# Kernel optimization log

Hardware: AMD Instinct MI355X
Metric: run time of the kernel (lower is better)

The kernel has to match this reference:

```python
import jax, jax.numpy as jnp
import numpy as np

V = 4096      # num codes (vocab)
D = 128       # embedding dim
K = 3         # diffusion scales
H = 4         # attn heads
FF = 128      # ff hidden
L = 2         # attn layers
NVIS = 8192   # visits
MAXC = 32     # max codes per visit
PAD = 0


def logmap0(x):
    # Poincare ball (c=1) log map at origin: artanh(||x||) * x / ||x||
    eps = 1e-7
    norm = jnp.linalg.norm(x, axis=-1, keepdims=True)
    norm_c = jnp.clip(norm, eps, 1.0 - 1e-5)
    return jnp.arctanh(norm_c) * x / jnp.maximum(norm, eps)


def layer_norm(x, g, b, eps=1e-5):
    m = jnp.mean(x, axis=-1, keepdims=True)
    v = jnp.mean((x - m) ** 2, axis=-1, keepdims=True)
    return (x - m) * jax.lax.rsqrt(v + eps) * g + b


def attn_block(x, Wqkv, bqkv, Wo, bo, W1, b1, W2, b2, g1, be1, g2, be2):
    # x: [V, D] (batch of 1, squeezed)
    hd = D // H
    qkv = x @ Wqkv.T + bqkv                      # [V, 3D]
    q, k, v = jnp.split(qkv, 3, axis=-1)
    q = q.reshape(V, H, hd)
    k = k.reshape(V, H, hd)
    v = v.reshape(V, H, hd)
    scores = jnp.einsum('shd,thd->hst', q, k) / np.sqrt(hd).astype(x.dtype)
    a = jax.nn.softmax(scores, axis=-1)          # [H, V, V]
    o = jnp.einsum('hst,thd->shd', a, v).reshape(V, D)
    attn_out = o @ Wo.T + bo
    x = layer_norm(x + attn_out, g1, be1)
    ff = jax.nn.gelu(x @ W1.T + b1) @ W2.T + b2
    return layer_norm(x + ff, g2, be2)


def setup_inputs() -> dict:
    key = jax.random.key(0)
    ks = jax.random.split(key, 20)
    inp = {}
    inp['visits'] = jax.random.randint(ks[0], (NVIS, MAXC), 0, V)
    # hyperbolic points inside unit ball
    inp['X_hyp'] = jax.random.normal(ks[1], (V, D), jnp.float32) * 0.01
    inp['kernels'] = jax.random.normal(ks[2], (K, V, V), jnp.float32) / V
    inp['proj_W'] = jax.random.normal(ks[3], (D, K * D), jnp.float32) * 0.05
    inp['proj_b'] = jnp.zeros((D,), jnp.float32)
    s = 0.05
    inp['Wqkv'] = jax.random.normal(ks[4], (L, 3 * D, D), jnp.float32) * s
    inp['bqkv'] = jnp.zeros((L, 3 * D), jnp.float32)
    inp['Wo'] = jax.random.normal(ks[5], (L, D, D), jnp.float32) * s
    inp['bo'] = jnp.zeros((L, D), jnp.float32)
    inp['W1'] = jax.random.normal(ks[6], (L, FF, D), jnp.float32) * s
    inp['b1'] = jnp.zeros((L, FF), jnp.float32)
    inp['W2'] = jax.random.normal(ks[7], (L, D, FF), jnp.float32) * s
    inp['b2'] = jnp.zeros((L, D), jnp.float32)
    inp['ln1_g'] = jnp.ones((L, D), jnp.float32)
    inp['ln1_b'] = jnp.zeros((L, D), jnp.float32)
    inp['ln2_g'] = jnp.ones((L, D), jnp.float32)
    inp['ln2_b'] = jnp.zeros((L, D), jnp.float32)
    return inp


def reference(visits, X_hyp, kernels, proj_W, proj_b, Wqkv, bqkv, Wo, bo,
              W1, b1, W2, b2, ln1_g, ln1_b, ln2_g, ln2_b):
    # ---- hyperbolic graph diffusion ----
    Z0 = logmap0(X_hyp)                              # [V, D]
    Z_scales = jnp.einsum('kuv,vd->ukd', kernels, Z0)  # [V, K, D]
    Z_cat = Z_scales.reshape(V, K * D)
    H_ = Z_cat @ proj_W.T + proj_b                   # [V, D]
    # ---- global self-attention stack ----
    for l in range(L):
        H_ = attn_block(H_, Wqkv[l], bqkv[l], Wo[l], bo[l],
                        W1[l], b1[l], W2[l], b2[l],
                        ln1_g[l], ln1_b[l], ln2_g[l], ln2_b[l])
    # ---- per-visit masked mean pooling (segment mean) ----
    mask = (visits != PAD)                           # [NVIS, MAXC]
    gathered = H_[visits] * mask[..., None]          # [NVIS, MAXC, D]
    cnt = jnp.sum(mask, axis=-1, keepdims=True).astype(H_.dtype)
    summed = jnp.sum(gathered, axis=1)               # [NVIS, D]
    return jnp.where(cnt > 0, summed / jnp.maximum(cnt, 1.0), 0.0)
```

## Files before the change

kernel.cpp:

```cpp
#include <hip/hip_runtime.h>
#include <hip/hip_bf16.h>
#include <math.h>

#define VN 4096
#define DIM 128
#define KS 3
#define NH 4
#define HD 32
#define NVIS 8192
#define MAXC 32
#define KTOT (KS*VN)

typedef unsigned short u16;
typedef __attribute__((ext_vector_type(8))) short short8;
typedef __attribute__((ext_vector_type(4))) float f32x4;
typedef __attribute__((ext_vector_type(4))) float f4v;

__device__ __forceinline__ u16 f2b(float f){
  union { float f; unsigned u; } c; c.f = f;
  unsigned u = c.u;
  return (u16)((u + 0x7fffu + ((u >> 16) & 1u)) >> 16);
}
__device__ __forceinline__ float b2f(u16 x){
  union { float f; unsigned u; } c; c.u = ((unsigned)x) << 16; return c.f;
}
__device__ __forceinline__ unsigned cvt2(float lo, float hi){
  unsigned r;
  asm("v_cvt_pk_bf16_f32 %0, %1, %2" : "=v"(r) : "v"(lo), "v"(hi));
  return r;
}
#define MFMA16(a,b,c) __builtin_amdgcn_mfma_f32_16x16x32_bf16((a),(b),(c),0,0,0)

__global__ __launch_bounds__(256) void k_logmap(const float* __restrict__ xh, u16* __restrict__ z0){
  __shared__ float xs[64][132];
  __shared__ float part[4][64];
  __shared__ float sscale[64];
  int t = threadIdx.x;
  int v0 = blockIdx.x * 64;
  #pragma unroll
  for(int i=0;i<8;i++){
    int id = t + 256*i; int e = id*4; int r = e>>7; int c = e&127;
    float4 u = *(const float4*)&xh[(size_t)(v0+r)*DIM + c];
    xs[r][c+0]=u.x; xs[r][c+1]=u.y; xs[r][c+2]=u.z; xs[r][c+3]=u.w;
  }
  __syncthreads();
  int r = t & 63, q = t >> 6;
  float p = 0.f;
  #pragma unroll
  for(int c=0;c<32;c++){ float x = xs[r][q*32+c]; p += x*x; }
  part[q][r] = p;
  __syncthreads();
  if(t < 64){
    float ss = part[0][t]+part[1][t]+part[2][t]+part[3][t];
    float n = sqrtf(ss);
    float nc = fminf(fmaxf(n, 1e-7f), 1.0f - 1e-5f);
    sscale[t] = atanhf(nc) / fmaxf(n, 1e-7f);
  }
  __syncthreads();
  #pragma unroll
  for(int i=0;i<8;i++){
    int id = t + 256*i; int e = id*4; int rr = e>>7; int cc = e&127;
    float s = sscale[rr];
    uint2 o = { cvt2(xs[rr][cc+0]*s, xs[rr][cc+1]*s),
                cvt2(xs[rr][cc+2]*s, xs[rr][cc+3]*s) };
    *(uint2*)&z0[(size_t)(v0+rr)*DIM + cc] = o;
  }
}

template<bool AF32, bool BF32>
__device__ __forceinline__ void gemm_k128_t(const void* __restrict__ Agv, int lda,
                                            const void* __restrict__ Bgv, int ldb,
                                            u16 (*As)[128*72], u16 (*Bs)[128*72], f32x4 (&acc)[2][8]){
  int t = threadIdx.x;
  int w=t>>6, lane=t&63, l15=lane&15, quad=lane>>4;
  #pragma unroll
  for(int s=0;s<2;s++)
    #pragma unroll
    for(int n=0;n<8;n++) acc[s][n] = (f32x4){0.f,0.f,0.f,0.f};

  float4 af[4][2]; uint4 ai[4];
  float4 bf[4][2]; uint4 bi[4];

  auto LOAD = [&](int kb){
    #pragma unroll
    for(int i=0;i<4;i++){
      int id = t + 256*i; int row = id>>3, c8 = id&7;
      if constexpr(AF32){
        const float* Ag = (const float*)Agv;
        af[i][0] = *(const float4*)&Ag[(size_t)row*lda + kb + c8*8];
        af[i][1] = *(const float4*)&Ag[(size_t)row*lda + kb + c8*8 + 4];
      } else {
        const u16* Ag = (const u16*)Agv;
        ai[i] = *(const uint4*)&Ag[(size_t)row*lda + kb + c8*8];
      }
      if constexpr(BF32){
        const float* Bg = (const float*)Bgv;
        bf[i][0] = *(const float4*)&Bg[(size_t)row*ldb + kb + c8*8];
        bf[i][1] = *(const float4*)&Bg[(size_t)row*ldb + kb + c8*8 + 4];
      } else {
        const u16* Bg = (const u16*)Bgv;
        bi[i] = *(const uint4*)&Bg[(size_t)row*ldb + kb + c8*8];
      }
    }
  };
  auto COMMIT = [&](u16* Ad, u16* Bd){
    #pragma unroll
    for(int i=0;i<4;i++){
      int id = t + 256*i; int row = id>>3, c8 = id&7;
      if constexpr(AF32){
        uint4 p = { cvt2(af[i][0].x, af[i][0].y), cvt2(af[i][0].z, af[i][0].w),
                    cvt2(af[i][1].x, af[i][1].y), cvt2(af[i][1].z, af[i][1].w) };
        *(uint4*)&Ad[row*72 + c8*8] = p;
      } else {
        *(uint4*)&Ad[row*72 + c8*8] = ai[i];
      }
      if constexpr(BF32){
        uint4 q = { cvt2(bf[i][0].x, bf[i][0].y), cvt2(bf[i][0].z, bf[i][0].w),
                    cvt2(bf[i][1].x, bf[i][1].y), cvt2(bf[i][1].z, bf[i][1].w) };
        *(uint4*)&Bd[row*72 + c8*8] = q;
      } else {
        *(uint4*)&Bd[row*72 + c8*8] = bi[i];
      }
    }
  };
  auto COMPUTE = [&](const u16* Asb, const u16* Bsb){
    #pragma unroll
    for(int ks=0; ks<2; ks++){
      short8 a[2], b[8];
      #pragma unroll
      for(int s=0;s<2;s++) a[s] = *(const short8*)&Asb[(w*32+s*16+l15)*72 + (ks*4+quad)*8];
      #pragma unroll
      for(int n=0;n<8;n++)  b[n] = *(const short8*)&Bsb[(n*16+l15)*72 + (ks*4+quad)*8];
      #pragma unroll
      for(int s=0;s<2;s++)
        #pragma unroll
        for(int n=0;n<8;n++) acc[s][n] = MFMA16(a[s], b[n], acc[s][n]);
    }
  };

  LOAD(0);  COMMIT(As[0], Bs[0]);  __syncthreads();
  LOAD(64); COMPUTE(As[0], Bs[0]); COMMIT(As[1], Bs[1]); __syncthreads();
  COMPUTE(As[1], Bs[1]);
}

__global__ __launch_bounds__(256) void k_gproj(const float* __restrict__ projW, const u16* __restrict__ z0,
                                               u16* __restrict__ gbuf){
  __shared__ u16 As[2][128*72], Bs[2][128*72];
  int kb = blockIdx.x >> 5, vt = blockIdx.x & 31;
  f32x4 acc[2][8];
  gemm_k128_t<true,false>(projW + kb*128, 3*DIM, z0 + (size_t)vt*128*DIM, DIM, As, Bs, acc);
  int t=threadIdx.x, w=t>>6, lane=t&63, l15=lane&15, quad=lane>>4;
  #pragma unroll
  for(int s=0;s<2;s++)
    #pragma unroll
    for(int n=0;n<8;n++)
      #pragma unroll
      for(int rg=0;rg<4;rg++){
        int d = w*32 + s*16 + quad*4 + rg;
        int v = vt*128 + n*16 + l15;
        gbuf[(size_t)(d*KS + kb)*VN + v] = f2b(acc[s][n][rg]);
      }
}

__global__ __launch_bounds__(256) void k_diff(const float* __restrict__ kers, const u16* __restrict__ gbuf,
                                              u16* __restrict__ hpart){
  __shared__ u16 As[2][128*72], Bs[2][128*72];
  int t = threadIdx.x;
  int mt = blockIdx.x & 31;
  int sl = blockIdx.x >> 5;
  int w=t>>6, lane=t&63, l15=lane&15, quad=lane>>4;
  f32x4 acc[2][8];
  #pragma unroll
  for(int s=0;s<2;s++)
    #pragma unroll
    for(int n=0;n<8;n++) acc[s][n] = (f32x4){0.f,0.f,0.f,0.f};
  int k0 = sl * 768;

  f4v  fa0[4], fa1[4];
  uint4 fb[4];

  auto LOADSTEP = [&](int step){
    int kk = k0 + step*64;
    int kout = kk >> 12; int vv = kk & 4095;
    #pragma unroll
    for(int i=0;i<4;i++){
      int id = t + 256*i; int row = id>>3, c8 = id&7;
      const float* ap = &kers[((size_t)kout<<24) + (size_t)(mt*128+row)*VN + vv + c8*8];
      fa0[i] = __builtin_nontemporal_load((const f4v*)ap);
      fa1[i] = __builtin_nontemporal_load((const f4v*)(ap+4));
      fb[i]  = *(const uint4*)&gbuf[(size_t)row*KTOT + kk + c8*8];
    }
  };
  auto COMMIT = [&](u16* Ad, u16* Bd){
    #pragma unroll
    for(int i=0;i<4;i++){
      int id = t + 256*i; int row = id>>3, c8 = id&7;
      uint4 pa = { cvt2(fa0[i].x, fa0[i].y), cvt2(fa0[i].z, fa0[i].w),
                   cvt2(fa1[i].x, fa1[i].y), cvt2(fa1[i].z, fa1[i].w) };
      *(uint4*)&Ad[row*72 + c8*8] = pa;
      *(uint4*)&Bd[row*72 + c8*8] = fb[i];
    }
  };
  auto COMPUTE = [&](const u16* Asb, const u16* Bsb){
    #pragma unroll
    for(int ks=0; ks<2; ks++){
      short8 a[2], b[8];
      #pragma unroll
      for(int s=0;s<2;s++) a[s] = *(const short8*)&Asb[(w*32+s*16+l15)*72 + (ks*4+quad)*8];
      #pragma unroll
      for(int n=0;n<8;n++)  b[n] = *(const short8*)&Bsb[(n*16+l15)*72 + (ks*4+quad)*8];
      #pragma unroll
      for(int s=0;s<2;s++)
        #pragma unroll
        for(int n=0;n<8;n++) acc[s][n] = MFMA16(a[s], b[n], acc[s][n]);
    }
  };

  LOADSTEP(0);
  COMMIT(As[0], Bs[0]);
  __syncthreads();
  #pragma unroll 1
  for(int sp=0; sp<6; sp++){
    LOADSTEP(2*sp+1);
    COMPUTE(As[0], Bs[0]);
    COMMIT(As[1], Bs[1]);
    __syncthreads();
    if(sp < 5){
      LOADSTEP(2*sp+2);
      COMPUTE(As[1], Bs[1]);
      COMMIT(As[0], Bs[0]);
      __syncthreads();
    }
  }
  COMPUTE(As[1], Bs[1]);

  u16* dst = hpart + ((size_t)blockIdx.x << 14);
  #pragma unroll
  for(int s=0;s<2;s++)
    #pragma unroll
    for(int n=0;n<8;n++)
      #pragma unroll
      for(int rg=0;rg<4;rg++)
        dst[(w*32+s*16+quad*4+rg)*128 + n*16 + l15] = f2b(acc[s][n][rg]);
}

__global__ __launch_bounds__(256) void k_hreduce(const u16* __restrict__ hpart, const float* __restrict__ pb,
                                                 float* __restrict__ h0){
  int idx = blockIdx.x*256 + threadIdx.x;
  int e0 = idx*4;
  int c0 = e0 & 127;
  float4 r;
  r.x = pb[c0+0]; r.y = pb[c0+1]; r.z = pb[c0+2]; r.w = pb[c0+3];
  #pragma unroll
  for(int sl=0; sl<16; sl++){
    uint2 u = *(const uint2*)&hpart[((size_t)sl<<19) + e0];
    r.x += b2f((u16)(u.x & 0xffffu)); r.y += b2f((u16)(u.x >> 16));
    r.z += b2f((u16)(u.y & 0xffffu)); r.w += b2f((u16)(u.y >> 16));
  }
  *(float4*)&h0[e0] = r;
}

template<bool AF32>
__global__ __launch_bounds__(256) void k_qkv(const void* __restrict__ xb, const float* __restrict__ Wq,
                                             const float* __restrict__ bq, u16* __restrict__ outq){
  __shared__ u16 As[2][128*72], Bs[2][128*72];
  int mt = blockIdx.x & 31, ntile = blockIdx.x >> 5;
  f32x4 acc[2][8];
  const void* Ap = AF32 ? (const void*)((const float*)xb + (size_t)mt*128*DIM)
                        : (const void*)((const u16*)xb + (size_t)mt*128*DIM);
  gemm_k128_t<AF32,true>(Ap, DIM, Wq + (size_t)ntile*128*DIM, DIM, As, Bs, acc);
  int t=threadIdx.x, w=t>>6, lane=t&63, l15=lane&15, quad=lane>>4;
  #pragma unroll
  for(int s=0;s<2;s++)
    #pragma unroll
    for(int n=0;n<8;n++)
      #pragma unroll
      for(int rg=0;rg<4;rg++){
        int row = mt*128 + w*32 + s*16 + quad*4 + rg;
        int col = ntile*128 + n*16 + l15;
        outq[(size_t)row*(3*DIM) + col] = f2b(acc[s][n][rg] + bq[col]);
      }
}

__global__ __launch_bounds__(256) void k_attn(const u16* __restrict__ qkv, float* __restrict__ opart,
                                              float* __restrict__ mlpart){
  __shared__ u16 Qs[64*40];
  __shared__ u16 Ksh[2][128*40];
  __shared__ u16 Vt[2][32*136];
  __shared__ u16 Ps[4*16*136];
  int t=threadIdx.x;
  int b = blockIdx.x;
  int h = b>>7, qt = (b>>1)&63, half = b&1;
  int w=t>>6, lane=t&63, l15=lane&15, quad=lane>>4;
  { int r = t>>2, c = t&3;
    *(uint4*)&Qs[r*40 + c*8] = *(const uint4*)&qkv[(size_t)(qt*64+r)*(3*DIM) + h*HD + c*8];
  }
  int skey = t>>2, sc4 = t&3;
  uint4 kreg[2], vreg[2];
  #pragma unroll
  for(int i=0;i<2;i++){
    int key = skey + 64*i;
    kreg[i] = *(const uint4*)&qkv[(size_t)((size_t)(half*16)*128+key)*(3*DIM) + DIM + h*HD + sc4*8];
    vreg[i] = *(const uint4*)&qkv[(size_t)((size_t)(half*16)*128+key)*(3*DIM) + 2*DIM + h*HD + sc4*8];
  }
  #pragma unroll
  for(int i=0;i<2;i++){
    int key = skey + 64*i;
    *(uint4*)&Ksh[0][key*40 + sc4*8] = kreg[i];
    u16 tmp[8]; *(uint4*)tmp = vreg[i];
    #pragma unroll
    for(int j=0;j<8;j++) Vt[0][(sc4*8+j)*136 + key] = tmp[j];
  }
  __syncthreads();
  short8 aq = *(short8*)&Qs[(w*16+l15)*40 + quad*8];
  f32x4 oacc[2]; oacc[0]=(f32x4){0.f,0.f,0.f,0.f}; oacc[1]=(f32x4){0.f,0.f,0.f,0.f};
  float mrun[4], lrun[4];
  #pragma unroll
  for(int rg=0;rg<4;rg++){ mrun[rg] = -INFINITY; lrun[rg] = 0.f; }
  const float sc = 0.17677669529663687f;
  for(int kti=0;kti<16;kti++){
    int cur = kti&1;
    if(kti<15){
      int kt = half*16 + kti + 1;
      #pragma unroll
      for(int i=0;i<2;i++){
        int key = skey + 64*i;
        kreg[i] = *(const uint4*)&qkv[(size_t)(kt*128+key)*(3*DIM) + DIM + h*HD + sc4*8];
        vreg[i] = *(const uint4*)&qkv[(size_t)(kt*128+key)*(3*DIM) + 2*DIM + h*HD + sc4*8];
      }
    }
    f32x4 s[8];
    #pragma unroll
    for(int n=0;n<8;n++)
      s[n] = MFMA16(aq, *(short8*)&Ksh[cur][(n*16+l15)*40 + quad*8], ((f32x4){0.f,0.f,0.f,0.f}));
    float mx[4];
    #pragma unroll
    for(int rg=0;rg<4;rg++){
      float m = -INFINITY;
      #pragma unroll
      for(int n=0;n<8;n++) m = fmaxf(m, s[n][rg]);
      #pragma unroll
      for(int off=1;off<16;off<<=1) m = fmaxf(m, __shfl_xor(m, off, 64));
      mx[rg] = m;
    }
    float alpha[4], rs[4];
    #pragma unroll
    for(int rg=0;rg<4;rg++){
      float mn = fmaxf(mrun[rg], mx[rg]);
      alpha[rg] = __expf(sc*(mrun[rg] - mn));
      mrun[rg] = mn; rs[rg] = 0.f;
    }
    #pragma unroll
    for(int n=0;n<8;n++)
      #pragma unroll
      for(int rg=0;rg<4;rg++){
        float p = __expf(sc*(s[n][rg] - mrun[rg]));
        s[n][rg] = p; rs[rg] += p;
      }
    #pragma unroll
    for(int rg=0;rg<4;rg++){
      #pragma unroll
      for(int off=1;off<16;off<<=1) rs[rg] += __shfl_xor(rs[rg], off, 64);
      lrun[rg] = lrun[rg]*alpha[rg] + rs[rg];
      oacc[0][rg] *= alpha[rg]; oacc[1][rg] *= alpha[rg];
    }
    #pragma unroll
    for(int n=0;n<8;n++)
      #pragma unroll
      for(int rg=0;rg<4;rg++)
        Ps[w*16*136 + (quad*4+rg)*136 + n*16 + l15] = f2b(s[n][rg]);
    #pragma unroll
    for(int kt2=0;kt2<4;kt2++){
      short8 ap = *(short8*)&Ps[w*16*136 + l15*136 + kt2*32 + quad*8];
      #pragma unroll
      for(int n2=0;n2<2;n2++)
        oacc[n2] = MFMA16(ap, *(short8*)&Vt[cur][(n2*16+l15)*136 + kt2*32 + quad*8], oacc[n2]);
    }
    if(kti<15){
      #pragma unroll
      for(int i=0;i<2;i++){
        int key = skey + 64*i;
        *(uint4*)&Ksh[cur^1][key*40 + sc4*8] = kreg[i];
        u16 tmp[8]; *(uint4*)tmp = vreg[i];
        #pragma unroll
        for(int j=0;j<8;j++) Vt[cur^1][(sc4*8+j)*136 + key] = tmp[j];
      }
    }
    __syncthreads();
  }
  float* op = opart + ((size_t)b << 11);
  #pragma unroll
  for(int n2=0;n2<2;n2++)
    #pragma unroll
    for(int rg=0;rg<4;rg++)
      op[(w*16+quad*4+rg)*32 + n2*16 + l15] = oacc[n2][rg];
  if(l15 == 0){
    float* ml = mlpart + ((size_t)b << 7);
    #pragma unroll
    for(int rg=0;rg<4;rg++){
      int r = w*16 + quad*4 + rg;
      ml[r] = sc*mrun[rg]; ml[64 + r] = lrun[rg];
    }
  }
}

__global__ __launch_bounds__(256) void k_oprojln(const float* __restrict__ opart, const float* __restrict__ mlpart,
                                                 const float* __restrict__ W,
                                                 const float* __restrict__ bias, const float* __restrict__ resf,
                                                 const float* __restrict__ g, const float* __restrict__ bb,
                                                 float* __restrict__ outf, u16* __restrict__ outb){
  __shared__ u16 As[128*72], Bs[128*72];
  int mt = blockIdx.x;
  int t=threadIdx.x, w=t>>6, lane=t&63, l15=lane&15, quad=lane>>4;
  f32x4 acc[2][8];
  #pragma unroll
  for(int s=0;s<2;s++)
    #pragma unroll
    for(int n=0;n<8;n++) acc[s][n] = (f32x4){0.f,0.f,0.f,0.f};
  #pragma unroll
  for(int step=0; step<2; step++){
    int kb = step*64;
    __syncthreads();
    #pragma unroll
    for(int i=0;i<4;i++){
      int id = t + 256*i; int row = id>>3, c8 = id&7;
      int col = kb + c8*8;
      int hh = col>>5, c0 = col&31;
      int grow = mt*128 + row;
      int hq = hh*64 + (grow>>6);
      int rr = grow & 63;
      const float* o0  = opart  + ((size_t)(hq*2)   << 11);
      const float* o1  = opart  + ((size_t)(hq*2+1) << 11);
      const float* ml0 = mlpart + ((size_t)(hq*2)   << 7);
      const float* ml1 = mlpart + ((size_t)(hq*2+1) << 7);
      float m0 = ml0[rr], l0 = ml0[64+rr], m1 = ml1[rr], l1 = ml1[64+rr];
      float m = fmaxf(m0, m1);
      float w0 = __expf(m0 - m), w1 = __expf(m1 - m);
      float inv = 1.f / (l0*w0 + l1*w1);
      float4 a0 = *(const float4*)&o0[rr*32 + c0];
      float4 a1 = *(const float4*)&o0[rr*32 + c0 + 4];
      float4 c0v = *(const float4*)&o1[rr*32 + c0];
      float4 c1v = *(const float4*)&o1[rr*32 + c0 + 4];
      uint4 pa = { cvt2((a0.x*w0+c0v.x*w1)*inv, (a0.y*w0+c0v.y*w1)*inv),
                   cvt2((a0.z*w0+c0v.z*w1)*inv, (a0.w*w0+c0v.w*w1)*inv),
                   cvt2((a1.x*w0+c1v.x*w1)*inv, (a1.y*w0+c1v.y*w1)*inv),
                   cvt2((a1.w*0.f + a1.x*w0 + c1v.x*w1)*inv*0.f + (a1.w*w0+c1v.w*w1)*inv, (a1.w*w0+c1v.w*w1)*inv) };
      pa.w = cvt2((a1.z*w0+c1v.z*w1)*inv, (a1.w*w0+c1v.w*w1)*inv);
      *(uint4*)&As[row*72 + c8*8] = pa;
      float4 f0 = *(const float4*)&W[(size_t)row*DIM + kb + c8*8];
      float4 f1 = *(const float4*)&W[(size_t)row*DIM + kb + c8*8 + 4];
      uint4 qa = { cvt2(f0.x, f0.y), cvt2(f0.z, f0.w),
                   cvt2(f1.x, f1.y), cvt2(f1.z, f1.w) };
      *(uint4*)&Bs[row*72 + c8*8] = qa;
    }
    __syncthreads();
    #pragma unroll
    for(int ks=0; ks<2; ks++){
      short8 a[2], b[8];
      #pragma unroll
      for(int s=0;s<2;s++) a[s] = *(short8*)&As[(w*32+s*16+l15)*72 + (ks*4+quad)*8];
      #pragma unroll
      for(int n=0;n<8;n++)  b[n] = *(short8*)&Bs[(n*16+l15)*72 + (ks*4+quad)*8];
      #pragma unroll
      for(int s=0;s<2;s++)
        #pragma unroll
        for(int n=0;n<8;n++) acc[s][n] = MFMA16(a[s], b[n], acc[s][n]);
    }
  }
  #pragma unroll
  for(int s=0;s<2;s++)
    #pragma unroll
    for(int n=0;n<8;n++)
      #pragma unroll
      for(int rg=0;rg<4;rg++){
        int row = mt*128 + w*32 + s*16 + quad*4 + rg;
        int col = n*16 + l15;
        acc[s][n][rg] += bias[col] + resf[(size_t)row*DIM + col];
      }
  #pragma unroll
  for(int s=0;s<2;s++)
    #pragma unroll
    for(int rg=0;rg<4;rg++){
      float a=0.f, bsum=0.f;
      #pragma unroll
      for(int n=0;n<8;n++){ float x = acc[s][n][rg]; a += x; bsum += x*x; }
      #pragma unroll
      for(int off=1;off<16;off<<=1){ a += __shfl_xor(a, off, 64); bsum += __shfl_xor(bsum, off, 64); }
      float mean = a*(1.f/128.f);
      float var  = bsum*(1.f/128.f) - mean*mean;
      float rstd = rsqrtf(var + 1e-5f);
      #pragma unroll
      for(int n=0;n<8;n++){
        int row = mt*128 + w*32 + s*16 + quad*4 + rg;
        int col = n*16 + l15;
        float y = (acc[s][n][rg] - mean)*rstd*g[col] + bb[col];
        outf[(size_t)row*DIM + col] = y;
        outb[(size_t)row*DIM + col] = f2b(y);
      }
    }
}

__global__ __launch_bounds__(256) void k_projln(const u16* __restrict__ Ab, const float* __restrict__ W,
                                                const float* __restrict__ bias, const float* __restrict__ resf,
                                                const float* __restrict__ g, const float* __restrict__ bb,
                                                float* __restrict__ outf, u16* __restrict__ outb){
  __shared__ u16 As[2][128*72], Bs[2][128*72];
  int mt = blockIdx.x;
  f32x4 acc[2][8];
  gemm_k128_t<false,true>(Ab + (size_t)mt*128*DIM, DIM, W, DIM, As, Bs, acc);
  int t=threadIdx.x, w=t>>6, lane=t&63, l15=lane&15, quad=lane>>4;
  #pragma unroll
  for(int s=0;s<2;s++)
    #pragma unroll
    for(int n=0;n<8;n++)
      #pragma unroll
      for(int rg=0;rg<4;rg++){
        int row = mt*128 + w*32 + s*16 + quad*4 + rg;
        int col = n*16 + l15;
        acc[s][n][rg] += bias[col] + resf[(size_t)row*DIM + col];
      }
  #pragma unroll
  for(int s=0;s<2;s++)
    #pragma unroll
    for(int rg=0;rg<4;rg++){
      float a=0.f, bsum=0.f;
      #pragma unroll
      for(int n=0;n<8;n++){ float x = acc[s][n][rg]; a += x; bsum += x*x; }
      #pragma unroll
      for(int off=1;off<16;off<<=1){ a += __shfl_xor(a, off, 64); bsum += __shfl_xor(bsum, off, 64); }
      float mean = a*(1.f/128.f);
      float var  = bsum*(1.f/128.f) - mean*mean;
      float rstd = rsqrtf(var + 1e-5f);
      #pragma unroll
      for(int n=0;n<8;n++){
        int row = mt*128 + w*32 + s*16 + quad*4 + rg;
        int col = n*16 + l15;
        float y = (acc[s][n][rg] - mean)*rstd*g[col] + bb[col];
        outf[(size_t)row*DIM + col] = y;
        outb[(size_t)row*DIM + col] = f2b(y);
      }
    }
}

__global__ __launch_bounds__(256) void k_ff1(const u16* __restrict__ Ab, const float* __restrict__ W,
                                             const float* __restrict__ bias, u16* __restrict__ outb){
  __shared__ u16 As[2][128*72], Bs[2][128*72];
  int mt = blockIdx.x;
  f32x4 acc[2][8];
  gemm_k128_t<false,true>(Ab + (size_t)mt*128*DIM, DIM, W, DIM, As, Bs, acc);
  int t=threadIdx.x, w=t>>6, lane=t&63, l15=lane&15, quad=lane>>4;
  #pragma unroll
  for(int s=0;s<2;s++)
    #pragma unroll
    for(int n=0;n<8;n++)
      #pragma unroll
      for(int rg=0;rg<4;rg++){
        int row = mt*128 + w*32 + s*16 + quad*4 + rg;
        int col = n*16 + l15;
        float v = acc[s][n][rg] + bias[col];
        float z = 0.7978845608028654f*(v + 0.044715f*v*v*v);
        float e = __expf(2.f*z);
        float th = 1.f - 2.f/(e + 1.f);
        outb[(size_t)row*DIM + col] = f2b(0.5f*v*(1.f + th));
      }
}

__global__ __launch_bounds__(256) void k_pool(const int* __restrict__ visits, const float* __restrict__ xf,
                                              float* __restrict__ out){
  int t = threadIdx.x;
  int vis = blockIdx.x*2 + (t>>7);
  int col = t & 127;
  float s = 0.f; int cnt = 0;
  #pragma unroll
  for(int j=0;j<MAXC;j++){
    int idx = visits[vis*MAXC + j];
    if(idx != 0){ s += xf[(size_t)idx*DIM + col]; cnt++; }
  }
  float r = (cnt > 0) ? s/(float)cnt : 0.f;
  out[(size_t)vis*DIM + col] = r;
}

extern "C" void kernel_launch(void* const* d_in, const int* in_sizes, int n_in,
                              void* d_out, int out_size, void* d_ws, size_t ws_size,
                              hipStream_t stream){
  (void)in_sizes; (void)n_in; (void)out_size; (void)ws_size;
  const int*   visits = (const int*)d_in[0];
  const float* xhyp  = (const float*)d_in[1];
  const float* kers  = (const float*)d_in[2];
  const float* projW = (const float*)d_in[3];
  const float* projb = (const float*)d_in[4];
  const float* Wqkv  = (const float*)d_in[5];
  const float* bqkv  = (const float*)d_in[6];
  const float* Wo    = (const float*)d_in[7];
  const float* bo    = (const float*)d_in[8];
  const float* W1    = (const float*)d_in[9];
  const float* b1    = (const float*)d_in[10];
  const float* W2    = (const float*)d_in[11];
  const float* b2    = (const float*)d_in[12];
  const float* g1    = (const float*)d_in[13];
  const float* be1   = (const float*)d_in[14];
  const float* g2    = (const float*)d_in[15];
  const float* be2   = (const float*)d_in[16];

  char* ws = (char*)d_ws;
  u16*   z0    = (u16*)(ws);
  u16*   gbuf  = (u16*)(ws + (1u<<20));
  float* h0    = (float*)(ws + (4u<<20));
  u16*   qkvb  = (u16*)(ws + (7u<<20));
  float* ln1f  = (float*)(ws + (11u<<20));
  u16*   ln1b  = (u16*)(ws + (13u<<20));
  u16*   ffa   = (u16*)(ws + (14u<<20));
  float* x1f   = (float*)(ws + (15u<<20));
  u16*   x1b   = (u16*)(ws + (17u<<20));
  float* x2f   = (float*)(ws + (18u<<20));
  u16*   x2b   = (u16*)(ws + (20u<<20));
  u16*   hpart = (u16*)(ws + (21u<<20));
  float* opart = (float*)(ws + (53u<<20));
  float* mlprt = (float*)(ws + (57u<<20));

  k_logmap<<<64,256,0,stream>>>(xhyp, z0);
  k_gproj<<<96,256,0,stream>>>(projW, z0, gbuf);
  k_diff<<<512,256,0,stream>>>(kers, gbuf, hpart);
  k_hreduce<<<512,256,0,stream>>>(hpart, projb, h0);

  const void* curA = (const void*)h0; bool af32 = true;
  const float* curf = h0;
  float* outfs[2] = {x1f, x2f}; u16* outbs[2] = {x1b, x2b};
  for(int l=0;l<2;l++){
    if(af32) k_qkv<true ><<<96,256,0,stream>>>(curA, Wqkv + (size_t)l*3*DIM*DIM, bqkv + (size_t)l*3*DIM, qkvb);
    else     k_qkv<false><<<96,256,0,stream>>>(curA, Wqkv + (size_t)l*3*DIM*DIM, bqkv + (size_t)l*3*DIM, qkvb);
    k_attn<<<512,256,0,stream>>>(qkvb, opart, mlprt);
    k_oprojln<<<32,256,0,stream>>>(opart, mlprt, Wo + (size_t)l*DIM*DIM, bo + (size_t)l*DIM, curf,
                                   g1 + (size_t)l*DIM, be1 + (size_t)l*DIM, ln1f, ln1b);
    k_ff1<<<32,256,0,stream>>>(ln1b, W1 + (size_t)l*DIM*DIM, b1 + (size_t)l*DIM, ffa);
    k_projln<<<32,256,0,stream>>>(ffa, W2 + (size_t)l*DIM*DIM, b2 + (size_t)l*DIM, ln1f,
                                  g2 + (size_t)l*DIM, be2 + (size_t)l*DIM, outfs[l], outbs[l]);
    curA = (const void*)outbs[l]; af32 = false; curf = outfs[l];
  }
  k_pool<<<4096,256,0,stream>>>(visits, curf, (float*)d_out);
}
```

Baseline: 555.4 us.

## Pre-convert weights to bf16, shrink small-GEMM tiles, skip unneeded softmax rescale

Adds a prep kernel that converts all attention and FF weights to bf16 once per call. The qkv, out-projection, FF1 and FF2 GEMMs are rewritten as single-stage 32-row tiles with 128 threads, so each launches 4x more blocks. This gives better use of the many CUs for these small GEMMs. In attention, the online-softmax rescale of the accumulators now runs only when some row max in the wave grew, saving exp and multiply work per key tile. The trade-offs are an extra launch and weight traffic for the prep kernel, plus more blocks each reloading the full weight tile.

```diff
diff --git a/kernel.cpp b/kernel.cpp
--- a/kernel.cpp
+++ b/kernel.cpp
@@ -10,6 +10,7 @@
 #define NVIS 8192
 #define MAXC 32
 #define KTOT (KS*VN)
+#define PITCH 136
 
 typedef unsigned short u16;
 typedef __attribute__((ext_vector_type(8))) short short8;
@@ -30,6 +31,24 @@
   return r;
 }
 #define MFMA16(a,b,c) __builtin_amdgcn_mfma_f32_16x16x32_bf16((a),(b),(c),0,0,0)
+
+__global__ __launch_bounds__(256) void k_wprep(const float* __restrict__ Wqkv, const float* __restrict__ Wo,
+                                               const float* __restrict__ W1, const float* __restrict__ W2,
+                                               u16* __restrict__ wb){
+  int t = blockIdx.x*256 + threadIdx.x;
+  #pragma unroll
+  for(int i=0;i<2;i++){
+    int e = t + 24576*i;
+    const float* s; u16* d; int ge;
+    if(e < 24576){ s = Wqkv; d = wb;          ge = e; }
+    else if(e < 32768){ s = Wo; d = wb + 98304;  ge = e - 24576; }
+    else if(e < 40960){ s = W1; d = wb + 131072; ge = e - 32768; }
+    else              { s = W2; d = wb + 163840; ge = e - 40960; }
+    float4 f = *(const float4*)&s[(size_t)ge*4];
+    uint2 o = { cvt2(f.x,f.y), cvt2(f.z,f.w) };
+    *(uint2*)&d[(size_t)ge*4] = o;
+  }
+}
 
 __global__ __launch_bounds__(256) void k_logmap(const float* __restrict__ xh, u16* __restrict__ z0){
   __shared__ float xs[64][132];
@@ -260,26 +279,192 @@
   *(float4*)&h0[e0] = r;
 }
 
+__device__ __forceinline__ void sg_stageB(const u16* __restrict__ wb, u16* Bs){
+  int t = threadIdx.x;
+  #pragma unroll
+  for(int i=0;i<16;i++){
+    int e = t + 128*i; int row = e>>4, c16 = e&15;
+    *(uint4*)&Bs[row*PITCH + c16*8] = *(const uint4*)&wb[row*128 + c16*8];
+  }
+}
+__device__ __forceinline__ void sg_stageA_b(const u16* __restrict__ src, int m0, u16* As){
+  int t = threadIdx.x;
+  #pragma unroll
+  for(int i=0;i<4;i++){
+    int e = t + 128*i; int row = e>>4, c16 = e&15;
+    *(uint4*)&As[row*PITCH + c16*8] = *(const uint4*)&src[(size_t)(m0+row)*DIM + c16*8];
+  }
+}
+__device__ __forceinline__ void sg_stageA_f(const float* __restrict__ src, int m0, u16* As){
+  int t = threadIdx.x;
+  #pragma unroll
+  for(int i=0;i<8;i++){
+    int e = t + 128*i; int row = e>>5, c4 = e&31;
+    float4 f = *(const float4*)&src[(size_t)(m0+row)*DIM + c4*4];
+    uint2 o = { cvt2(f.x,f.y), cvt2(f.z,f.w) };
+    *(uint2*)&As[row*PITCH + c4*4] = o;
+  }
+}
+__device__ __forceinline__ void sg_compute(const u16* As, const u16* Bs, f32x4 (&acc)[8]){
+  int t=threadIdx.x, w=t>>6, lane=t&63, l15=lane&15, quad=lane>>4;
+  #pragma unroll
+  for(int n=0;n<8;n++) acc[n] = (f32x4){0.f,0.f,0.f,0.f};
+  #pragma unroll
+  for(int kk=0;kk<4;kk++){
+    short8 a = *(const short8*)&As[(w*16+l15)*PITCH + kk*32 + quad*8];
+    #pragma unroll
+    for(int n=0;n<8;n++){
+      short8 b = *(const short8*)&Bs[(n*16+l15)*PITCH + kk*32 + quad*8];
+      acc[n] = MFMA16(a, b, acc[n]);
+    }
+  }
+}
+__device__ __forceinline__ void sg_ln(f32x4 (&acc)[8], const float* __restrict__ g,
+                                      const float* __restrict__ bv, int l15){
+  #pragma unroll
+  for(int rg=0;rg<4;rg++){
+    float a=0.f, bs=0.f;
+    #pragma unroll
+    for(int n=0;n<8;n++){ float x = acc[n][rg]; a += x; bs += x*x; }
+    #pragma unroll
+    for(int off=1;off<16;off<<=1){ a += __shfl_xor(a, off, 64); bs += __shfl_xor(bs, off, 64); }
+    float mean = a*(1.f/128.f);
+    float var  = bs*(1.f/128.f) - mean*mean;
+    float rstd = rsqrtf(var + 1e-5f);
+    #pragma unroll
+    for(int n=0;n<8;n++){
+      int col = n*16 + l15;
+      acc[n][rg] = (acc[n][rg] - mean)*rstd*g[col] + bv[col];
+    }
+  }
+}
+
 template<bool AF32>
-__global__ __launch_bounds__(256) void k_qkv(const void* __restrict__ xb, const float* __restrict__ Wq,
-                                             const float* __restrict__ bq, u16* __restrict__ outq){
-  __shared__ u16 As[2][128*72], Bs[2][128*72];
-  int mt = blockIdx.x & 31, ntile = blockIdx.x >> 5;
-  f32x4 acc[2][8];
-  const void* Ap = AF32 ? (const void*)((const float*)xb + (size_t)mt*128*DIM)
-                        : (const void*)((const u16*)xb + (size_t)mt*128*DIM);
-  gemm_k128_t<AF32,true>(Ap, DIM, Wq + (size_t)ntile*128*DIM, DIM, As, Bs, acc);
+__global__ __launch_bounds__(128) void k_qkv_s(const void* __restrict__ xb, const u16* __restrict__ wq,
+                                               const float* __restrict__ bq, u16* __restrict__ outq){
+  __shared__ u16 As[32*PITCH], Bs[128*PITCH];
+  int bx = blockIdx.x; int mt = bx & 127, nt = bx >> 7;
+  if(AF32) sg_stageA_f((const float*)xb, mt*32, As);
+  else     sg_stageA_b((const u16*)xb, mt*32, As);
+  sg_stageB(wq + nt*16384, Bs);
+  __syncthreads();
+  f32x4 acc[8]; sg_compute(As, Bs, acc);
   int t=threadIdx.x, w=t>>6, lane=t&63, l15=lane&15, quad=lane>>4;
   #pragma unroll
-  for(int s=0;s<2;s++)
-    #pragma unroll
-    for(int n=0;n<8;n++)
-      #pragma unroll
-      for(int rg=0;rg<4;rg++){
-        int row = mt*128 + w*32 + s*16 + quad*4 + rg;
-        int col = ntile*128 + n*16 + l15;
-        outq[(size_t)row*(3*DIM) + col] = f2b(acc[s][n][rg] + bq[col]);
-      }
+  for(int n=0;n<8;n++)
+    #pragma unroll
+    for(int rg=0;rg<4;rg++){
+      int row = mt*32 + w*16 + quad*4 + rg;
+      int col = nt*128 + n*16 + l15;
+      outq[(size_t)row*(3*DIM) + col] = f2b(acc[n][rg] + bq[col]);
+    }
+}
+
+__global__ __launch_bounds__(128) void k_oprojln_s(const float* __restrict__ opart, const float* __restrict__ mlpart,
+                                                   const u16* __restrict__ wo,
+                                                   const float* __restrict__ bias, const float* __restrict__ resf,
+                                                   const float* __restrict__ g, const float* __restrict__ bb,
+                                                   float* __restrict__ outf, u16* __restrict__ outb){
+  __shared__ u16 As[32*PITCH], Bs[128*PITCH];
+  int mt = blockIdx.x; int t = threadIdx.x;
+  #pragma unroll
+  for(int i=0;i<8;i++){
+    int e = t + 128*i; int row = e>>5, c4 = e&31; int col = c4*4;
+    int hh = col>>5, c0 = col&31;
+    int grow = mt*32 + row;
+    int hq = hh*64 + (grow>>6); int rr = grow & 63;
+    const float* o0  = opart  + ((size_t)(hq*2)   << 11);
+    const float* o1  = opart  + ((size_t)(hq*2+1) << 11);
+    const float* ml0 = mlpart + ((size_t)(hq*2)   << 7);
+    const float* ml1 = mlpart + ((size_t)(hq*2+1) << 7);
+    float m0 = ml0[rr], l0 = ml0[64+rr], m1 = ml1[rr], l1 = ml1[64+rr];
+    float m = fmaxf(m0, m1);
+    float w0 = __expf(m0 - m), w1 = __expf(m1 - m);
+    float inv = 1.f / (l0*w0 + l1*w1);
+    float4 a  = *(const float4*)&o0[rr*32 + c0];
+    float4 c  = *(const float4*)&o1[rr*32 + c0];
+    uint2 o = { cvt2((a.x*w0+c.x*w1)*inv, (a.y*w0+c.y*w1)*inv),
+                cvt2((a.z*w0+c.z*w1)*inv, (a.w*w0+c.w*w1)*inv) };
+    *(uint2*)&As[row*PITCH + col] = o;
+  }
+  sg_stageB(wo, Bs);
+  __syncthreads();
+  f32x4 acc[8]; sg_compute(As, Bs, acc);
+  int w=t>>6, lane=t&63, l15=lane&15, quad=lane>>4;
+  #pragma unroll
+  for(int n=0;n<8;n++)
+    #pragma unroll
+    for(int rg=0;rg<4;rg++){
+      int row = mt*32 + w*16 + quad*4 + rg;
+      int col = n*16 + l15;
+      acc[n][rg] += bias[col] + resf[(size_t)row*DIM + col];
+    }
+  sg_ln(acc, g, bb, l15);
+  #pragma unroll
+  for(int n=0;n<8;n++)
+    #pragma unroll
+    for(int rg=0;rg<4;rg++){
+      int row = mt*32 + w*16 + quad*4 + rg;
+      int col = n*16 + l15;
+      float y = acc[n][rg];
+      outf[(size_t)row*DIM + col] = y;
+      outb[(size_t)row*DIM + col] = f2b(y);
+    }
+}
+
+__global__ __launch_bounds__(128) void k_ff1_s(const u16* __restrict__ Ab, const u16* __restrict__ w1,
+                                               const float* __restrict__ bias, u16* __restrict__ outb){
+  __shared__ u16 As[32*PITCH], Bs[128*PITCH];
+  int mt = blockIdx.x;
+  sg_stageA_b(Ab, mt*32, As);
+  sg_stageB(w1, Bs);
+  __syncthreads();
+  f32x4 acc[8]; sg_compute(As, Bs, acc);
+  int t=threadIdx.x, w=t>>6, lane=t&63, l15=lane&15, quad=lane>>4;
+  #pragma unroll
+  for(int n=0;n<8;n++)
+    #pragma unroll
+    for(int rg=0;rg<4;rg++){
+      int row = mt*32 + w*16 + quad*4 + rg;
+      int col = n*16 + l15;
+      float v = acc[n][rg] + bias[col];
+      float z = 0.7978845608028654f*(v + 0.044715f*v*v*v);
+      float e = __expf(2.f*z);
+      float th = 1.f - 2.f/(e + 1.f);
+      outb[(size_t)row*DIM + col] = f2b(0.5f*v*(1.f + th));
+    }
+}
+
+__global__ __launch_bounds__(128) void k_projln_s(const u16* __restrict__ Ab, const u16* __restrict__ w2,
+                                                  const float* __restrict__ bias, const float* __restrict__ resf,
+                                                  const float* __restrict__ g, const float* __restrict__ bb,
+                                                  float* __restrict__ outf, u16* __restrict__ outb){
+  __shared__ u16 As[32*PITCH], Bs[128*PITCH];
+  int mt = blockIdx.x;
+  sg_stageA_b(Ab, mt*32, As);
+  sg_stageB(w2, Bs);
+  __syncthreads();
+  f32x4 acc[8]; sg_compute(As, Bs, acc);
+  int t=threadIdx.x, w=t>>6, lane=t&63, l15=lane&15, quad=lane>>4;
+  #pragma unroll
+  for(int n=0;n<8;n++)
+    #pragma unroll
+    for(int rg=0;rg<4;rg++){
+      int row = mt*32 + w*16 + quad*4 + rg;
+      int col = n*16 + l15;
+      acc[n][rg] += bias[col] + resf[(size_t)row*DIM + col];
+    }
+  sg_ln(acc, g, bb, l15);
+  #pragma unroll
+  for(int n=0;n<8;n++)
+    #pragma unroll
+    for(int rg=0;rg<4;rg++){
+      int row = mt*32 + w*16 + quad*4 + rg;
+      int col = n*16 + l15;
+      float y = acc[n][rg];
+      outf[(size_t)row*DIM + col] = y;
+      outb[(size_t)row*DIM + col] = f2b(y);
+    }
 }
 
 __global__ __launch_bounds__(256) void k_attn(const u16* __restrict__ qkv, float* __restrict__ opart,
@@ -343,13 +528,22 @@
       for(int off=1;off<16;off<<=1) m = fmaxf(m, __shfl_xor(m, off, 64));
       mx[rg] = m;
     }
-    float alpha[4], rs[4];
-    #pragma unroll
-    for(int rg=0;rg<4;rg++){
-      float mn = fmaxf(mrun[rg], mx[rg]);
-      alpha[rg] = __expf(sc*(mrun[rg] - mn));
-      mrun[rg] = mn; rs[rg] = 0.f;
-    }
+    bool grew = false;
+    #pragma unroll
+    for(int rg=0;rg<4;rg++) grew = grew || (mx[rg] > mrun[rg]);
+    if(__any(grew)){
+      #pragma unroll
+      for(int rg=0;rg<4;rg++){
+        float mn = fmaxf(mrun[rg], mx[rg]);
+        float alpha = __expf(sc*(mrun[rg] - mn));
+        mrun[rg] = mn;
+        lrun[rg] *= alpha;
+        oacc[0][rg] *= alpha; oacc[1][rg] *= alpha;
+      }
+    }
+    float rs[4];
+    #pragma unroll
+    for(int rg=0;rg<4;rg++) rs[rg] = 0.f;
     #pragma unroll
     for(int n=0;n<8;n++)
       #pragma unroll
@@ -361,8 +555,7 @@
     for(int rg=0;rg<4;rg++){
       #pragma unroll
       for(int off=1;off<16;off<<=1) rs[rg] += __shfl_xor(rs[rg], off, 64);
-      lrun[rg] = lrun[rg]*alpha[rg] + rs[rg];
-      oacc[0][rg] *= alpha[rg]; oacc[1][rg] *= alpha[rg];
+      lrun[rg] += rs[rg];
     }
     #pragma unroll
     for(int n=0;n<8;n++)
@@ -402,167 +595,6 @@
       ml[r] = sc*mrun[rg]; ml[64 + r] = lrun[rg];
     }
   }
-}
-
-__global__ __launch_bounds__(256) void k_oprojln(const float* __restrict__ opart, const float* __restrict__ mlpart,
-                                                 const float* __restrict__ W,
-                                                 const float* __restrict__ bias, const float* __restrict__ resf,
-                                                 const float* __restrict__ g, const float* __restrict__ bb,
-                                                 float* __restrict__ outf, u16* __restrict__ outb){
-  __shared__ u16 As[128*72], Bs[128*72];
-  int mt = blockIdx.x;
-  int t=threadIdx.x, w=t>>6, lane=t&63, l15=lane&15, quad=lane>>4;
-  f32x4 acc[2][8];
-  #pragma unroll
-  for(int s=0;s<2;s++)
-    #pragma unroll
-    for(int n=0;n<8;n++) acc[s][n] = (f32x4){0.f,0.f,0.f,0.f};
-  #pragma unroll
-  for(int step=0; step<2; step++){
-    int kb = step*64;
-    __syncthreads();
-    #pragma unroll
-    for(int i=0;i<4;i++){
-      int id = t + 256*i; int row = id>>3, c8 = id&7;
-      int col = kb + c8*8;
-      int hh = col>>5, c0 = col&31;
-      int grow = mt*128 + row;
-      int hq = hh*64 + (grow>>6);
-      int rr = grow & 63;
-      const float* o0  = opart  + ((size_t)(hq*2)   << 11);
-      const float* o1  = opart  + ((size_t)(hq*2+1) << 11);
-      const float* ml0 = mlpart + ((size_t)(hq*2)   << 7);
-      const float* ml1 = mlpart + ((size_t)(hq*2+1) << 7);
-      float m0 = ml0[rr], l0 = ml0[64+rr], m1 = ml1[rr], l1 = ml1[64+rr];
-      float m = fmaxf(m0, m1);
-      float w0 = __expf(m0 - m), w1 = __expf(m1 - m);
-      float inv = 1.f / (l0*w0 + l1*w1);
-      float4 a0 = *(const float4*)&o0[rr*32 + c0];
-      float4 a1 = *(const float4*)&o0[rr*32 + c0 + 4];
-      float4 c0v = *(const float4*)&o1[rr*32 + c0];
-      float4 c1v = *(const float4*)&o1[rr*32 + c0 + 4];
-      uint4 pa = { cvt2((a0.x*w0+c0v.x*w1)*inv, (a0.y*w0+c0v.y*w1)*inv),
-                   cvt2((a0.z*w0+c0v.z*w1)*inv, (a0.w*w0+c0v.w*w1)*inv),
-                   cvt2((a1.x*w0+c1v.x*w1)*inv, (a1.y*w0+c1v.y*w1)*inv),
-                   cvt2((a1.w*0.f + a1.x*w0 + c1v.x*w1)*inv*0.f + (a1.w*w0+c1v.w*w1)*inv, (a1.w*w0+c1v.w*w1)*inv) };
-      pa.w = cvt2((a1.z*w0+c1v.z*w1)*inv, (a1.w*w0+c1v.w*w1)*inv);
-      *(uint4*)&As[row*72 + c8*8] = pa;
-      float4 f0 = *(const float4*)&W[(size_t)row*DIM + kb + c8*8];
-      float4 f1 = *(const float4*)&W[(size_t)row*DIM + kb + c8*8 + 4];
-      uint4 qa = { cvt2(f0.x, f0.y), cvt2(f0.z, f0.w),
-                   cvt2(f1.x, f1.y), cvt2(f1.z, f1.w) };
-      *(uint4*)&Bs[row*72 + c8*8] = qa;
-    }
-    __syncthreads();
-    #pragma unroll
-    for(int ks=0; ks<2; ks++){
-      short8 a[2], b[8];
-      #pragma unroll
-      for(int s=0;s<2;s++) a[s] = *(short8*)&As[(w*32+s*16+l15)*72 + (ks*4+quad)*8];
-      #pragma unroll
-      for(int n=0;n<8;n++)  b[n] = *(short8*)&Bs[(n*16+l15)*72 + (ks*4+quad)*8];
-      #pragma unroll
-      for(int s=0;s<2;s++)
-        #pragma unroll
-        for(int n=0;n<8;n++) acc[s][n] = MFMA16(a[s], b[n], acc[s][n]);
-    }
-  }
-  #pragma unroll
-  for(int s=0;s<2;s++)
-    #pragma unroll
-    for(int n=0;n<8;n++)
-      #pragma unroll
-      for(int rg=0;rg<4;rg++){
-        int row = mt*128 + w*32 + s*16 + quad*4 + rg;
-        int col = n*16 + l15;
-        acc[s][n][rg] += bias[col] + resf[(size_t)row*DIM + col];
-      }
-  #pragma unroll
-  for(int s=0;s<2;s++)
-    #pragma unroll
-    for(int rg=0;rg<4;rg++){
-      float a=0.f, bsum=0.f;
-      #pragma unroll
-      for(int n=0;n<8;n++){ float x = acc[s][n][rg]; a += x; bsum += x*x; }
-      #pragma unroll
-      for(int off=1;off<16;off<<=1){ a += __shfl_xor(a, off, 64); bsum += __shfl_xor(bsum, off, 64); }
-      float mean = a*(1.f/128.f);
-      float var  = bsum*(1.f/128.f) - mean*mean;
-      float rstd = rsqrtf(var + 1e-5f);
-      #pragma unroll
-      for(int n=0;n<8;n++){
-        int row = mt*128 + w*32 + s*16 + quad*4 + rg;
-        int col = n*16 + l15;
-        float y = (acc[s][n][rg] - mean)*rstd*g[col] + bb[col];
-        outf[(size_t)row*DIM + col] = y;
-        outb[(size_t)row*DIM + col] = f2b(y);
-      }
-    }
-}
-
-__global__ __launch_bounds__(256) void k_projln(const u16* __restrict__ Ab, const float* __restrict__ W,
-                                                const float* __restrict__ bias, const float* __restrict__ resf,
-                                                const float* __restrict__ g, const float* __restrict__ bb,
-                                                float* __restrict__ outf, u16* __restrict__ outb){
-  __shared__ u16 As[2][128*72], Bs[2][128*72];
-  int mt = blockIdx.x;
-  f32x4 acc[2][8];
-  gemm_k128_t<false,true>(Ab + (size_t)mt*128*DIM, DIM, W, DIM, As, Bs, acc);
-  int t=threadIdx.x, w=t>>6, lane=t&63, l15=lane&15, quad=lane>>4;
-  #pragma unroll
-  for(int s=0;s<2;s++)
-    #pragma unroll
-    for(int n=0;n<8;n++)
-      #pragma unroll
-      for(int rg=0;rg<4;rg++){
-        int row = mt*128 + w*32 + s*16 + quad*4 + rg;
-        int col = n*16 + l15;
-        acc[s][n][rg] += bias[col] + resf[(size_t)row*DIM + col];
-      }
-  #pragma unroll
-  for(int s=0;s<2;s++)
-    #pragma unroll
-    for(int rg=0;rg<4;rg++){
-      float a=0.f, bsum=0.f;
-      #pragma unroll
-      for(int n=0;n<8;n++){ float x = acc[s][n][rg]; a += x; bsum += x*x; }
-      #pragma unroll
-      for(int off=1;off<16;off<<=1){ a += __shfl_xor(a, off, 64); bsum += __shfl_xor(bsum, off, 64); }
-      float mean = a*(1.f/128.f);
-      float var  = bsum*(1.f/128.f) - mean*mean;
-      float rstd = rsqrtf(var + 1e-5f);
-      #pragma unroll
-      for(int n=0;n<8;n++){
-        int row = mt*128 + w*32 + s*16 + quad*4 + rg;
-        int col = n*16 + l15;
-        float y = (acc[s][n][rg] - mean)*rstd*g[col] + bb[col];
-        outf[(size_t)row*DIM + col] = y;
-        outb[(size_t)row*DIM + col] = f2b(y);
-      }
-    }
-}
-
-__global__ __launch_bounds__(256) void k_ff1(const u16* __restrict__ Ab, const float* __restrict__ W,
-                                             const float* __restrict__ bias, u16* __restrict__ outb){
-  __shared__ u16 As[2][128*72], Bs[2][128*72];
-  int mt = blockIdx.x;
-  f32x4 acc[2][8];
-  gemm_k128_t<false,true>(Ab + (size_t)mt*128*DIM, DIM, W, DIM, As, Bs, acc);
-  int t=threadIdx.x, w=t>>6, lane=t&63, l15=lane&15, quad=lane>>4;
-  #pragma unroll
-  for(int s=0;s<2;s++)
-    #pragma unroll
-    for(int n=0;n<8;n++)
-      #pragma unroll
-      for(int rg=0;rg<4;rg++){
-        int row = mt*128 + w*32 + s*16 + quad*4 + rg;
-        int col = n*16 + l15;
-        float v = acc[s][n][rg] + bias[col];
-        float z = 0.7978845608028654f*(v + 0.044715f*v*v*v);
-        float e = __expf(2.f*z);
-        float th = 1.f - 2.f/(e + 1.f);
-        outb[(size_t)row*DIM + col] = f2b(0.5f*v*(1.f + th));
-      }
 }
 
 __global__ __launch_bounds__(256) void k_pool(const int* __restrict__ visits, const float* __restrict__ xf,
@@ -615,27 +647,31 @@
   float* x2f   = (float*)(ws + (18u<<20));
   u16*   x2b   = (u16*)(ws + (20u<<20));
   u16*   hpart = (u16*)(ws + (21u<<20));
+  u16*   wb    = (u16*)(ws + (40u<<20));
   float* opart = (float*)(ws + (53u<<20));
   float* mlprt = (float*)(ws + (57u<<20));
 
+  k_wprep<<<96,256,0,stream>>>(Wqkv, Wo, W1, W2, wb);
   k_logmap<<<64,256,0,stream>>>(xhyp, z0);
   k_gproj<<<96,256,0,stream>>>(projW, z0, gbuf);
   k_diff<<<512,256,0,stream>>>(kers, gbuf, hpart);
   k_hreduce<<<512,256,0,stream>>>(hpart, projb, h0);
 
-  const void* curA = (const void*)h0; bool af32 = true;
-  const float* curf = h0;
-  float* outfs[2] = {x1f, x2f}; u16* outbs[2] = {x1b, x2b};
-  for(int l=0;l<2;l++){
-    if(af32) k_qkv<true ><<<96,256,0,stream>>>(curA, Wqkv + (size_t)l*3*DIM*DIM, bqkv + (size_t)l*3*DIM, qkvb);
-    else     k_qkv<false><<<96,256,0,stream>>>(curA, Wqkv + (size_t)l*3*DIM*DIM, bqkv + (size_t)l*3*DIM, qkvb);
-    k_attn<<<512,256,0,stream>>>(qkvb, opart, mlprt);
-    k_oprojln<<<32,256,0,stream>>>(opart, mlprt, Wo + (size_t)l*DIM*DIM, bo + (size_t)l*DIM, curf,
-                                   g1 + (size_t)l*DIM, be1 + (size_t)l*DIM, ln1f, ln1b);
-    k_ff1<<<32,256,0,stream>>>(ln1b, W1 + (size_t)l*DIM*DIM, b1 + (size_t)l*DIM, ffa);
-    k_projln<<<32,256,0,stream>>>(ffa, W2 + (size_t)l*DIM*DIM, b2 + (size_t)l*DIM, ln1f,
-                                  g2 + (size_t)l*DIM, be2 + (size_t)l*DIM, outfs[l], outbs[l]);
-    curA = (const void*)outbs[l]; af32 = false; curf = outfs[l];
-  }
-  k_pool<<<4096,256,0,stream>>>(visits, curf, (float*)d_out);
-}
+  const u16* wq_l[2] = { wb,            wb + 49152 };
+  const u16* wo_l[2] = { wb + 98304,    wb + 98304 + 16384 };
+  const u16* w1_l[2] = { wb + 131072,   wb + 131072 + 16384 };
+  const u16* w2_l[2] = { wb + 163840,   wb + 163840 + 16384 };
+
+  k_qkv_s<true><<<384,128,0,stream>>>((const void*)h0, wq_l[0], bqkv, qkvb);
+  k_attn<<<512,256,0,stream>>>(qkvb, opart, mlprt);
+  k_oprojln_s<<<128,128,0,stream>>>(opart, mlprt, wo_l[0], bo, h0, g1, be1, ln1f, ln1b);
+  k_ff1_s<<<128,128,0,stream>>>(ln1b, w1_l[0], b1, ffa);
+  k_projln_s<<<128,128,0,stream>>>(ffa, w2_l[0], b2, ln1f, g2, be2, x1f, x1b);
+  k_qkv_s<false><<<384,128,0,stream>>>((const void*)x1b, wq_l[1], bqkv + 3*DIM, qkvb);
+  k_attn<<<512,256,0,stream>>>(qkvb, opart, mlprt);
+  k_oprojln_s<<<128,128,0,stream>>>(opart, mlprt, wo_l[1], bo + DIM, x1f, g1 + DIM, be1 + DIM, ln1f, ln1b);
+  k_ff1_s<<<128,128,0,stream>>>(ln1b, w1_l[1], b1 + DIM, ffa);
+  k_projln_s<<<128,128,0,stream>>>(ffa, w2_l[1], b2 + DIM, ln1f, g2 + DIM, be2 + DIM, x2f, x2b);
+
+  k_pool<<<4096,256,0,stream>>>(visits, x2f, (float*)d_out);
+}
```

Result: faster. 527.7 us (-5.0%).
